# Performance work log

Measured on AMD Instinct MI355X. Metric: run time of the kernel, lower is better.

Reference implementation:

```python
import jax, jax.numpy as jnp
import numpy as np

B, S, D, H = 2, 2048, 1024, 16
HEAD_DIM = D // H
MAX_REL = 64  # max_relative_position in source


def setup_inputs() -> dict:
    key = jax.random.key(0)
    ks = jax.random.split(key, 8)
    std = 0.02
    return {
        "query": jax.random.normal(ks[0], (B, S, D), jnp.float32),
        "key": jax.random.normal(ks[1], (B, S, D), jnp.float32),
        "value": jax.random.normal(ks[2], (B, S, D), jnp.float32),
        "attention_mask": jnp.zeros((B, 1, 1, S), jnp.float32),
        "Wq": jax.random.normal(ks[3], (D, D), jnp.float32) * std,
        "bq": jnp.zeros((D,), jnp.float32),
        "Wk": jax.random.normal(ks[4], (D, D), jnp.float32) * std,
        "bk": jnp.zeros((D,), jnp.float32),
        "Wv": jax.random.normal(ks[5], (D, D), jnp.float32) * std,
        "bv": jnp.zeros((D,), jnp.float32),
        "rel_table": jax.random.normal(ks[6], (2 * MAX_REL + 1, HEAD_DIM), jnp.float32) * std,
    }


def _split_heads(x, b):
    # [B,S,D] -> [B,H,S,d]
    return x.reshape(b, -1, H, HEAD_DIM).transpose(0, 2, 1, 3)


def reference(query, key, value, attention_mask, Wq, bq, Wk, bk, Wv, bv, rel_table):
    b, s, _ = query.shape
    q = _split_heads(query @ Wq + bq, b)   # [B,H,S,d]
    k = _split_heads(key @ Wk + bk, b)
    v = _split_heads(value @ Wv + bv, b)

    scores = jnp.einsum("bhqd,bhkd->bhqk", q, k)  # [B,H,S,S]

    # relative-position key bias: rel_k[q_idx, k_idx] = table[clip(k-q)+MAX_REL]
    idx = jnp.arange(s)
    dist = jnp.clip(idx[None, :] - idx[:, None], -MAX_REL, MAX_REL) + MAX_REL  # [S,S]
    rel_k = rel_table[dist]  # [S,S,d]
    scores = scores + jnp.einsum("bhqd,qkd->bhqk", q, rel_k)

    scores = scores / jnp.sqrt(jnp.asarray(HEAD_DIM, scores.dtype))
    scores = scores + attention_mask  # additive mask, broadcast [B,1,1,S]

    probs = jax.nn.softmax(scores, axis=-1)  # dropout is identity (p=0 / eval)
    ctx = jnp.einsum("bhqk,bhkd->bhqd", probs, v)
    ctx = ctx.transpose(0, 2, 1, 3).reshape(b, s, H * HEAD_DIM)
    return ctx
```

## Files before the change

kernel.cpp:

```cpp
#include <hip/hip_runtime.h>
#include <hip/hip_bf16.h>

#define BB 2
#define SS 2048
#define DD 1024
#define HH 16
#define HD 64
#define NREL 129
#define LOG2E 1.4426950408889634f
#define SCALEQ (LOG2E / 8.0f)
#define KVB 131072l

typedef short s8v __attribute__((ext_vector_type(8)));
typedef short s4v __attribute__((ext_vector_type(4)));
typedef float f4 __attribute__((ext_vector_type(4)));

#define MFMA_BF16 __builtin_amdgcn_mfma_f32_16x16x32_bf16

__device__ __forceinline__ float bf2f(unsigned short u) {
  union { unsigned int i; float f; } x; x.i = ((unsigned int)u) << 16; return x.f;
}
__device__ __forceinline__ unsigned short f2bf(float f) {
  union { float f; unsigned int i; } x; x.f = f;
  unsigned int r = x.i + 0x7fffu + ((x.i >> 16) & 1u);
  return (unsigned short)(r >> 16);
}
__device__ __forceinline__ unsigned int pk2bf(float a, float b) {
  union { __hip_bfloat162 h2; unsigned int u; } c;
  c.h2 = __float22bfloat162_rn(float2{a, b});
  return c.u;
}
__device__ __forceinline__ void gl_lds16(const void* g, void* l) {
  __builtin_amdgcn_global_load_lds(
      (const __attribute__((address_space(1))) unsigned int*)g,
      (__attribute__((address_space(3))) unsigned int*)l, 16, 0, 0);
}

__global__ __launch_bounds__(256) void cvt_x(
    const float* __restrict__ xq, const float* __restrict__ xk,
    const float* __restrict__ xv, unsigned short* __restrict__ xb) {
  const int z = blockIdx.y;
  const float* in = (z == 0) ? xq : (z == 1) ? xk : xv;
  unsigned short* out = xb + (long)z * 4096 * DD;
  const long i = ((long)blockIdx.x * 256 + threadIdx.x) * 8;
  f4 a = *(const f4*)(in + i);
  f4 b = *(const f4*)(in + i + 4);
  unsigned int u[4];
  u[0] = pk2bf(a[0], a[1]); u[1] = pk2bf(a[2], a[3]);
  u[2] = pk2bf(b[0], b[1]); u[3] = pk2bf(b[2], b[3]);
  *(s8v*)(out + i) = *(s8v*)u;
}

__global__ __launch_bounds__(256) void cvt_w(
    const float* __restrict__ Wq, const float* __restrict__ Wk,
    const float* __restrict__ Wv, unsigned short* __restrict__ WTt) {
  __shared__ unsigned short tile[64][72];
  const int z = blockIdx.z;
  const float* in = (z == 0) ? Wq : (z == 1) ? Wk : Wv;
  unsigned short* out = WTt + (long)z * 1048576;
  const int c0 = blockIdx.x * 64, r0 = blockIdx.y * 64;
  const int t = threadIdx.x;
  const int r = t >> 2;
  #pragma unroll
  for (int j = 0; j < 4; ++j) {
    int cc = (t & 3) * 16 + j * 4;
    f4 v = *(const f4*)(in + (long)(r0 + r) * DD + c0 + cc);
    #pragma unroll
    for (int e = 0; e < 4; ++e) tile[r][cc + e] = f2bf(v[e]);
  }
  __syncthreads();
  const int c = t >> 2;
  #pragma unroll
  for (int h = 0; h < 2; ++h) {
    int r8 = (t & 3) + 4 * h;
    unsigned short vals[8];
    #pragma unroll
    for (int j = 0; j < 8; ++j) vals[j] = tile[r8 * 8 + j][c];
    int n = c0 + c, kb = r0 + r8 * 8;
    long off = ((long)(n >> 7) * 131072) + ((kb >> 6) * 8192) +
               (((kb & 63) >> 3) * 1024) + ((n & 127) * 8);
    *(s8v*)(out + off) = *(s8v*)vals;
  }
}

__global__ __launch_bounds__(256, 4) void proj_gemm(
    const unsigned short* __restrict__ Xb, const unsigned short* __restrict__ WTt,
    const float* __restrict__ bq, const float* __restrict__ bk,
    const float* __restrict__ bv,
    unsigned short* __restrict__ qbuf, unsigned short* __restrict__ ktile,
    unsigned short* __restrict__ vtile) {
  __shared__ __align__(16) unsigned short wt[8][128][8];
  unsigned short* wtf = &wt[0][0][0];
  const int z = blockIdx.z;
  const unsigned short* X = Xb + (long)z * 4096 * DD;
  const unsigned short* WTz = WTt + (long)z * 1048576;
  const float* bias = (z == 0) ? bq : (z == 1) ? bk : bv;

  const int n0 = blockIdx.x * 128, m0 = blockIdx.y * 128;
  const int t = threadIdx.x, w = t >> 6, l = t & 63;
  const int lm = l & 15, qd = l >> 4;

  f4 acc[8][2];
  #pragma unroll
  for (int i = 0; i < 8; ++i) { acc[i][0] = (f4)0.0f; acc[i][1] = (f4)0.0f; }

  const unsigned short* x0 = X + (long)(m0 + w * 32 + lm) * DD;
  const unsigned short* x1 = x0 + 16 * DD;
  const unsigned short* wtile0 = WTz + (long)(n0 >> 7) * 131072;

  for (int k0 = 0; k0 < DD; k0 += 64) {
    __syncthreads();
    const unsigned short* tb = wtile0 + (k0 >> 6) * 8192;
    #pragma unroll
    for (int i = 0; i < 4; ++i) {
      int idx = w * 4 + i;
      gl_lds16(tb + idx * 512 + l * 8, wtf + idx * 512);
    }
    s8v a00 = *(const s8v*)(x0 + k0 + qd * 8);
    s8v a01 = *(const s8v*)(x0 + k0 + 32 + qd * 8);
    s8v a10 = *(const s8v*)(x1 + k0 + qd * 8);
    s8v a11 = *(const s8v*)(x1 + k0 + 32 + qd * 8);
    asm volatile("s_waitcnt vmcnt(0)" ::: "memory");
    __syncthreads();
    #pragma unroll
    for (int cb = 0; cb < 8; ++cb) {
      s8v b0 = *(const s8v*)&wt[qd][cb * 16 + lm][0];
      s8v b1 = *(const s8v*)&wt[4 + qd][cb * 16 + lm][0];
      acc[cb][0] = MFMA_BF16(a00, b0, acc[cb][0], 0, 0, 0);
      acc[cb][0] = MFMA_BF16(a01, b1, acc[cb][0], 0, 0, 0);
      acc[cb][1] = MFMA_BF16(a10, b0, acc[cb][1], 0, 0, 0);
      acc[cb][1] = MFMA_BF16(a11, b1, acc[cb][1], 0, 0, 0);
    }
  }
  if (z == 0) {
    #pragma unroll
    for (int cb = 0; cb < 8; ++cb) {
      int n = n0 + cb * 16 + lm;
      float bvv = bias[n];
      int hh = n >> 6, d = n & 63;
      #pragma unroll
      for (int ms = 0; ms < 2; ++ms) {
        #pragma unroll
        for (int r = 0; r < 4; ++r) {
          int m = m0 + w * 32 + ms * 16 + qd * 4 + r;
          int bidx = m >> 11, s = m & (SS - 1);
          qbuf[((long)(bidx * HH + hh) * SS + s) * HD + d] =
              f2bf((acc[cb][ms][r] + bvv) * SCALEQ);
        }
      }
    }
  } else if (z == 1) {
    #pragma unroll
    for (int cb = 0; cb < 8; ++cb) {
      int n = n0 + cb * 16 + lm;
      float bvv = bias[n];
      int hh = n >> 6, d = n & 63;
      int c = d >> 3, e = d & 7;
      #pragma unroll
      for (int ms = 0; ms < 2; ++ms) {
        #pragma unroll
        for (int r = 0; r < 4; ++r) {
          int m = m0 + w * 32 + ms * 16 + qd * 4 + r;
          int bidx = m >> 11, s = m & (SS - 1);
          long bh = bidx * HH + hh;
          ktile[bh * KVB + (s >> 6) * 4096 + c * 512 + (s & 63) * 8 + e] =
              f2bf(acc[cb][ms][r] + bvv);
        }
      }
    }
  } else {
    #pragma unroll
    for (int cb = 0; cb < 8; ++cb) {
      int n = n0 + cb * 16 + lm;
      float bvv = bias[n];
      int hh = n >> 6, d = n & 63;
      #pragma unroll
      for (int ms = 0; ms < 2; ++ms) {
        int m = m0 + w * 32 + ms * 16 + qd * 4;
        int bidx = m >> 11, s = m & (SS - 1);
        long bh = bidx * HH + hh;
        unsigned short o4[4];
        #pragma unroll
        for (int r = 0; r < 4; ++r) o4[r] = f2bf(acc[cb][ms][r] + bvv);
        *(s4v*)&vtile[bh * KVB + (s >> 6) * 4096 + ((s & 63) >> 3) * 512 +
                      d * 8 + (s & 7)] = *(s4v*)o4;
      }
    }
  }
}

__global__ __launch_bounds__(256, 2) void attn(
    const unsigned short* __restrict__ qb, const unsigned short* __restrict__ ktile,
    const unsigned short* __restrict__ vtile, const float* __restrict__ tableF,
    const float* __restrict__ maskF, float* __restrict__ out) {
  __shared__ __align__(16) unsigned short ks[2][8][64][8];
  __shared__ __align__(16) unsigned short vs[2][8][64][8];
  __shared__ __align__(16) unsigned short qr2[NREL][66];
  __shared__ __align__(16) unsigned short pbuf[4][16][40];
  __shared__ float mk[SS];

  const int bh = blockIdx.y, b = bh >> 4, h = bh & 15;
  const int q0 = blockIdx.x * 64;
  const int t = threadIdx.x, w = t >> 6, l = t & 63;
  const int lm = l & 15, qd = l >> 4;

  const unsigned short* kkb = ktile + (long)bh * KVB;
  const unsigned short* vvb = vtile + (long)bh * KVB;

  #pragma unroll
  for (int i = 0; i < 2; ++i) {
    int c = 2 * w + i;
    gl_lds16(kkb + c * 512 + l * 8, &ks[0][c][0][0]);
    gl_lds16(vvb + c * 512 + l * 8, &vs[0][c][0][0]);
  }

  {
    const float* mrow = maskF + b * SS;
    f4 m0v = *(const f4*)(mrow + t * 8);
    f4 m1v = *(const f4*)(mrow + t * 8 + 4);
    #pragma unroll
    for (int e = 0; e < 4; ++e) {
      mk[t * 8 + e] = m0v[e] * LOG2E;
      mk[t * 8 + 4 + e] = m1v[e] * LOG2E;
    }
  }

  const unsigned short* qrow = qb + ((long)bh * SS + q0 + w * 16 + lm) * HD;
  const s8v qa0 = *(const s8v*)(qrow + qd * 8);
  const s8v qa1 = *(const s8v*)(qrow + 32 + qd * 8);

  #pragma unroll
  for (int cb = 0; cb < 9; ++cb) {
    int dist = cb * 16 + lm;
    int dc = dist > NREL - 1 ? NREL - 1 : dist;
    const float* trow = tableF + dc * HD;
    f4 t0 = *(const f4*)(trow + qd * 8);
    f4 t1 = *(const f4*)(trow + qd * 8 + 4);
    f4 t2 = *(const f4*)(trow + 32 + qd * 8);
    f4 t3 = *(const f4*)(trow + 32 + qd * 8 + 4);
    unsigned int tb[8];
    tb[0] = pk2bf(t0[0], t0[1]); tb[1] = pk2bf(t0[2], t0[3]);
    tb[2] = pk2bf(t1[0], t1[1]); tb[3] = pk2bf(t1[2], t1[3]);
    tb[4] = pk2bf(t2[0], t2[1]); tb[5] = pk2bf(t2[2], t2[3]);
    tb[6] = pk2bf(t3[0], t3[1]); tb[7] = pk2bf(t3[2], t3[3]);
    s8v b0 = *(s8v*)tb, b1 = *(s8v*)(tb + 4);
    f4 c = MFMA_BF16(qa0, b0, (f4)0.0f, 0, 0, 0);
    c = MFMA_BF16(qa1, b1, c, 0, 0, 0);
    if (dist <= NREL - 1) {
      #pragma unroll
      for (int r = 0; r < 4; ++r)
        qr2[dist][w * 16 + qd * 4 + r] = f2bf(c[r]);
    }
  }
  asm volatile("s_waitcnt vmcnt(0)" ::: "memory");
  __syncthreads();

  const int qcol = w * 16 + lm;
  const float bLo = bf2f(qr2[0][qcol]);
  const float bHi = bf2f(qr2[128][qcol]);

  float m_ = -1e30f, l_ = 0.0f;
  f4 c4[4];
  #pragma unroll
  for (int i = 0; i < 4; ++i) c4[i] = (f4)0.0f;

  for (int rr = 0; rr < 32; ++rr) {
    const int kk = rr << 6;
    const int buf = rr & 1;
    if (rr < 31) {
      const int nb = buf ^ 1;
      const unsigned short* kg = kkb + (rr + 1) * 4096;
      const unsigned short* vg = vvb + (rr + 1) * 4096;
      #pragma unroll
      for (int i = 0; i < 2; ++i) {
        int c = 2 * w + i;
        gl_lds16(kg + c * 512 + l * 8, &ks[nb][c][0][0]);
        gl_lds16(vg + c * 512 + l * 8, &vs[nb][c][0][0]);
      }
    }
    f4 st[4];
    #pragma unroll
    for (int tt = 0; tt < 4; ++tt) {
      s8v k0v = *(const s8v*)&ks[buf][qd][tt * 16 + lm][0];
      s8v k1v = *(const s8v*)&ks[buf][4 + qd][tt * 16 + lm][0];
      st[tt] = MFMA_BF16(k0v, qa0, (f4)0.0f, 0, 0, 0);
      st[tt] = MFMA_BF16(k1v, qa1, st[tt], 0, 0, 0);
    }
    float z[16];
    const int kband = kk - q0;
    if (kband >= 128) {
      #pragma unroll
      for (int tt = 0; tt < 4; ++tt) {
        f4 mv = *(const f4*)&mk[kk + tt * 16 + qd * 4];
        #pragma unroll
        for (int r = 0; r < 4; ++r) z[tt * 4 + r] = st[tt][r] + bHi + mv[r];
      }
    } else if (kband <= -128) {
      #pragma unroll
      for (int tt = 0; tt < 4; ++tt) {
        f4 mv = *(const f4*)&mk[kk + tt * 16 + qd * 4];
        #pragma unroll
        for (int r = 0; r < 4; ++r) z[tt * 4 + r] = st[tt][r] + bLo + mv[r];
      }
    } else {
      const int dbb = kband - qcol + 64 + qd * 4;
      #pragma unroll
      for (int tt = 0; tt < 4; ++tt) {
        f4 mv = *(const f4*)&mk[kk + tt * 16 + qd * 4];
        #pragma unroll
        for (int r = 0; r < 4; ++r) {
          int d = dbb + tt * 16 + r;
          d = d < 0 ? 0 : (d > 128 ? 128 : d);
          z[tt * 4 + r] = st[tt][r] + bf2f(qr2[d][qcol]) + mv[r];
        }
      }
    }
    float tm = z[0];
    #pragma unroll
    for (int i = 1; i < 16; ++i) tm = fmaxf(tm, z[i]);
    tm = fmaxf(tm, __shfl_xor(tm, 16));
    tm = fmaxf(tm, __shfl_xor(tm, 32));
    float mn = fmaxf(m_, tm);
    float alpha = __builtin_amdgcn_exp2f(m_ - mn);
    m_ = mn;
    float p[16];
    #pragma unroll
    for (int i = 0; i < 16; ++i) p[i] = __builtin_amdgcn_exp2f(z[i] - mn);
    float ts = 0.0f;
    #pragma unroll
    for (int i = 0; i < 16; ++i) ts += p[i];
    ts += __shfl_xor(ts, 16);
    ts += __shfl_xor(ts, 32);
    l_ = l_ * alpha + ts;
    #pragma unroll
    for (int db = 0; db < 4; ++db)
      #pragma unroll
      for (int r = 0; r < 4; ++r) c4[db][r] *= alpha;

    *(unsigned int*)&pbuf[w][lm][qd * 4] = pk2bf(p[0], p[1]);
    *(unsigned int*)&pbuf[w][lm][qd * 4 + 2] = pk2bf(p[2], p[3]);
    *(unsigned int*)&pbuf[w][lm][16 + qd * 4] = pk2bf(p[4], p[5]);
    *(unsigned int*)&pbuf[w][lm][16 + qd * 4 + 2] = pk2bf(p[6], p[7]);
    asm volatile("s_waitcnt lgkmcnt(0)" ::: "memory");
    {
      s8v pa = *(const s8v*)&pbuf[w][lm][qd * 8];
      #pragma unroll
      for (int db = 0; db < 4; ++db) {
        s8v va = *(const s8v*)&vs[buf][qd][db * 16 + lm][0];
        c4[db] = MFMA_BF16(va, pa, c4[db], 0, 0, 0);
      }
    }
    *(unsigned int*)&pbuf[w][lm][qd * 4] = pk2bf(p[8], p[9]);
    *(unsigned int*)&pbuf[w][lm][qd * 4 + 2] = pk2bf(p[10], p[11]);
    *(unsigned int*)&pbuf[w][lm][16 + qd * 4] = pk2bf(p[12], p[13]);
    *(unsigned int*)&pbuf[w][lm][16 + qd * 4 + 2] = pk2bf(p[14], p[15]);
    asm volatile("s_waitcnt lgkmcnt(0)" ::: "memory");
    {
      s8v pb = *(const s8v*)&pbuf[w][lm][qd * 8];
      #pragma unroll
      for (int db = 0; db < 4; ++db) {
        s8v vb = *(const s8v*)&vs[buf][4 + qd][db * 16 + lm][0];
        c4[db] = MFMA_BF16(vb, pb, c4[db], 0, 0, 0);
      }
    }
    asm volatile("s_waitcnt vmcnt(0)" ::: "memory");
    __syncthreads();
  }

  const float inv = 1.0f / l_;
  float* obase = out + ((long)b * SS + q0 + qcol) * DD + h * HD;
  #pragma unroll
  for (int db = 0; db < 4; ++db) {
    f4 o;
    #pragma unroll
    for (int r = 0; r < 4; ++r) o[r] = c4[db][r] * inv;
    *(f4*)(obase + db * 16 + qd * 4) = o;
  }
}

extern "C" void kernel_launch(void* const* d_in, const int* in_sizes, int n_in,
                              void* d_out, int out_size, void* d_ws, size_t ws_size,
                              hipStream_t stream) {
  const float* query = (const float*)d_in[0];
  const float* key   = (const float*)d_in[1];
  const float* value = (const float*)d_in[2];
  const float* mask  = (const float*)d_in[3];
  const float* Wq    = (const float*)d_in[4];
  const float* bq    = (const float*)d_in[5];
  const float* Wk    = (const float*)d_in[6];
  const float* bk    = (const float*)d_in[7];
  const float* Wv    = (const float*)d_in[8];
  const float* bv    = (const float*)d_in[9];
  const float* table = (const float*)d_in[10];

  char* ws = (char*)d_ws;
  unsigned short* WTt   = (unsigned short*)(ws);
  unsigned short* Xb    = (unsigned short*)(ws + (8l << 20));
  unsigned short* qbuf  = (unsigned short*)(ws + (32l << 20));
  unsigned short* ktile = (unsigned short*)(ws + (40l << 20));
  unsigned short* vtile = (unsigned short*)(ws + (48l << 20));

  cvt_x<<<dim3(2048, 3, 1), 256, 0, stream>>>(query, key, value, Xb);

  cvt_w<<<dim3(16, 16, 3), 256, 0, stream>>>(Wq, Wk, Wv, WTt);

  proj_gemm<<<dim3(8, 32, 3), 256, 0, stream>>>(Xb, WTt, bq, bk, bv,
                                                qbuf, ktile, vtile);

  attn<<<dim3(32, 32, 1), 256, 0, stream>>>(qbuf, ktile, vtile, table, mask,
                                            (float*)d_out);
}
```

Measured before the change: 258.1 us.

## Process two 16-row query tiles per wave to reuse K/V fragments

Each wave now handles 32 query rows instead of 16, so the attention block covers 128 queries and the grid halves. K and V fragments read from LDS are reused across both query sub-tiles, which halves K/V global and LDS traffic per query and amortizes the loop sync overhead. The cost is more registers per thread (two accumulator sets and two score arrays), a larger relative-bias LDS table, and only 512 blocks, which may reduce occupancy and latency hiding.

New measurement: 234.9 us. 1.1x faster.

```diff
diff --git a/kernel.cpp b/kernel.cpp
--- a/kernel.cpp
+++ b/kernel.cpp
@@ -195,14 +195,16 @@
     const float* __restrict__ maskF, float* __restrict__ out) {
   __shared__ __align__(16) unsigned short ks[2][8][64][8];
   __shared__ __align__(16) unsigned short vs[2][8][64][8];
-  __shared__ __align__(16) unsigned short qr2[NREL][66];
+  __shared__ __align__(16) unsigned short qr2[NREL][130];
   __shared__ __align__(16) unsigned short pbuf[4][16][40];
   __shared__ float mk[SS];
 
   const int bh = blockIdx.y, b = bh >> 4, h = bh & 15;
-  const int q0 = blockIdx.x * 64;
+  const int q0 = blockIdx.x * 128;
   const int t = threadIdx.x, w = t >> 6, l = t & 63;
   const int lm = l & 15, qd = l >> 4;
+  const int qw = q0 + w * 32;
+  const int qc0 = w * 32 + lm, qc1 = qc0 + 16;
 
   const unsigned short* kkb = ktile + (long)bh * KVB;
   const unsigned short* vvb = vtile + (long)bh * KVB;
@@ -225,9 +227,11 @@
     }
   }
 
-  const unsigned short* qrow = qb + ((long)bh * SS + q0 + w * 16 + lm) * HD;
+  const unsigned short* qrow = qb + ((long)bh * SS + qw + lm) * HD;
   const s8v qa0 = *(const s8v*)(qrow + qd * 8);
   const s8v qa1 = *(const s8v*)(qrow + 32 + qd * 8);
+  const s8v qb0 = *(const s8v*)(qrow + 16 * HD + qd * 8);
+  const s8v qb1 = *(const s8v*)(qrow + 16 * HD + 32 + qd * 8);
 
   #pragma unroll
   for (int cb = 0; cb < 9; ++cb) {
@@ -244,25 +248,28 @@
     tb[4] = pk2bf(t2[0], t2[1]); tb[5] = pk2bf(t2[2], t2[3]);
     tb[6] = pk2bf(t3[0], t3[1]); tb[7] = pk2bf(t3[2], t3[3]);
     s8v b0 = *(s8v*)tb, b1 = *(s8v*)(tb + 4);
-    f4 c = MFMA_BF16(qa0, b0, (f4)0.0f, 0, 0, 0);
-    c = MFMA_BF16(qa1, b1, c, 0, 0, 0);
+    f4 c0 = MFMA_BF16(qa0, b0, (f4)0.0f, 0, 0, 0);
+    c0 = MFMA_BF16(qa1, b1, c0, 0, 0, 0);
+    f4 c1 = MFMA_BF16(qb0, b0, (f4)0.0f, 0, 0, 0);
+    c1 = MFMA_BF16(qb1, b1, c1, 0, 0, 0);
     if (dist <= NREL - 1) {
       #pragma unroll
-      for (int r = 0; r < 4; ++r)
-        qr2[dist][w * 16 + qd * 4 + r] = f2bf(c[r]);
+      for (int r = 0; r < 4; ++r) {
+        qr2[dist][w * 32 + qd * 4 + r] = f2bf(c0[r]);
+        qr2[dist][w * 32 + 16 + qd * 4 + r] = f2bf(c1[r]);
+      }
     }
   }
   asm volatile("s_waitcnt vmcnt(0)" ::: "memory");
   __syncthreads();
 
-  const int qcol = w * 16 + lm;
-  const float bLo = bf2f(qr2[0][qcol]);
-  const float bHi = bf2f(qr2[128][qcol]);
-
-  float m_ = -1e30f, l_ = 0.0f;
-  f4 c4[4];
-  #pragma unroll
-  for (int i = 0; i < 4; ++i) c4[i] = (f4)0.0f;
+  const float bLo0 = bf2f(qr2[0][qc0]), bHi0 = bf2f(qr2[128][qc0]);
+  const float bLo1 = bf2f(qr2[0][qc1]), bHi1 = bf2f(qr2[128][qc1]);
+
+  float m0_ = -1e30f, l0_ = 0.0f, m1_ = -1e30f, l1_ = 0.0f;
+  f4 c40[4], c41[4];
+  #pragma unroll
+  for (int i = 0; i < 4; ++i) { c40[i] = (f4)0.0f; c41[i] = (f4)0.0f; }
 
   for (int rr = 0; rr < 32; ++rr) {
     const int kk = rr << 6;
@@ -278,103 +285,156 @@
         gl_lds16(vg + c * 512 + l * 8, &vs[nb][c][0][0]);
       }
     }
-    f4 st[4];
+    f4 st0[4], st1[4];
     #pragma unroll
     for (int tt = 0; tt < 4; ++tt) {
       s8v k0v = *(const s8v*)&ks[buf][qd][tt * 16 + lm][0];
       s8v k1v = *(const s8v*)&ks[buf][4 + qd][tt * 16 + lm][0];
-      st[tt] = MFMA_BF16(k0v, qa0, (f4)0.0f, 0, 0, 0);
-      st[tt] = MFMA_BF16(k1v, qa1, st[tt], 0, 0, 0);
-    }
-    float z[16];
-    const int kband = kk - q0;
-    if (kband >= 128) {
+      st0[tt] = MFMA_BF16(k0v, qa0, (f4)0.0f, 0, 0, 0);
+      st0[tt] = MFMA_BF16(k1v, qa1, st0[tt], 0, 0, 0);
+      st1[tt] = MFMA_BF16(k0v, qb0, (f4)0.0f, 0, 0, 0);
+      st1[tt] = MFMA_BF16(k1v, qb1, st1[tt], 0, 0, 0);
+    }
+    float z0[16], z1[16];
+    const int kw = kk - qw;
+    if (kw >= 96) {
       #pragma unroll
       for (int tt = 0; tt < 4; ++tt) {
         f4 mv = *(const f4*)&mk[kk + tt * 16 + qd * 4];
         #pragma unroll
-        for (int r = 0; r < 4; ++r) z[tt * 4 + r] = st[tt][r] + bHi + mv[r];
-      }
-    } else if (kband <= -128) {
+        for (int r = 0; r < 4; ++r) {
+          z0[tt * 4 + r] = st0[tt][r] + bHi0 + mv[r];
+          z1[tt * 4 + r] = st1[tt][r] + bHi1 + mv[r];
+        }
+      }
+    } else if (kw <= -128) {
       #pragma unroll
       for (int tt = 0; tt < 4; ++tt) {
         f4 mv = *(const f4*)&mk[kk + tt * 16 + qd * 4];
         #pragma unroll
-        for (int r = 0; r < 4; ++r) z[tt * 4 + r] = st[tt][r] + bLo + mv[r];
+        for (int r = 0; r < 4; ++r) {
+          z0[tt * 4 + r] = st0[tt][r] + bLo0 + mv[r];
+          z1[tt * 4 + r] = st1[tt][r] + bLo1 + mv[r];
+        }
       }
     } else {
-      const int dbb = kband - qcol + 64 + qd * 4;
+      const int db0 = kw - lm + 64 + qd * 4;
       #pragma unroll
       for (int tt = 0; tt < 4; ++tt) {
         f4 mv = *(const f4*)&mk[kk + tt * 16 + qd * 4];
         #pragma unroll
         for (int r = 0; r < 4; ++r) {
-          int d = dbb + tt * 16 + r;
-          d = d < 0 ? 0 : (d > 128 ? 128 : d);
-          z[tt * 4 + r] = st[tt][r] + bf2f(qr2[d][qcol]) + mv[r];
+          int du = db0 + tt * 16 + r;
+          int d0 = du < 0 ? 0 : (du > 128 ? 128 : du);
+          int d1 = du - 16; d1 = d1 < 0 ? 0 : (d1 > 128 ? 128 : d1);
+          z0[tt * 4 + r] = st0[tt][r] + bf2f(qr2[d0][qc0]) + mv[r];
+          z1[tt * 4 + r] = st1[tt][r] + bf2f(qr2[d1][qc1]) + mv[r];
         }
       }
     }
-    float tm = z[0];
-    #pragma unroll
-    for (int i = 1; i < 16; ++i) tm = fmaxf(tm, z[i]);
-    tm = fmaxf(tm, __shfl_xor(tm, 16));
-    tm = fmaxf(tm, __shfl_xor(tm, 32));
-    float mn = fmaxf(m_, tm);
-    float alpha = __builtin_amdgcn_exp2f(m_ - mn);
-    m_ = mn;
-    float p[16];
-    #pragma unroll
-    for (int i = 0; i < 16; ++i) p[i] = __builtin_amdgcn_exp2f(z[i] - mn);
-    float ts = 0.0f;
-    #pragma unroll
-    for (int i = 0; i < 16; ++i) ts += p[i];
-    ts += __shfl_xor(ts, 16);
-    ts += __shfl_xor(ts, 32);
-    l_ = l_ * alpha + ts;
+    float tm0 = z0[0], tm1 = z1[0];
+    #pragma unroll
+    for (int i = 1; i < 16; ++i) {
+      tm0 = fmaxf(tm0, z0[i]);
+      tm1 = fmaxf(tm1, z1[i]);
+    }
+    tm0 = fmaxf(tm0, __shfl_xor(tm0, 16));
+    tm0 = fmaxf(tm0, __shfl_xor(tm0, 32));
+    tm1 = fmaxf(tm1, __shfl_xor(tm1, 16));
+    tm1 = fmaxf(tm1, __shfl_xor(tm1, 32));
+    float mn0 = fmaxf(m0_, tm0), mn1 = fmaxf(m1_, tm1);
+    float al0 = __builtin_amdgcn_exp2f(m0_ - mn0);
+    float al1 = __builtin_amdgcn_exp2f(m1_ - mn1);
+    m0_ = mn0; m1_ = mn1;
+    float s0 = 0.0f, s1 = 0.0f;
+    #pragma unroll
+    for (int i = 0; i < 16; ++i) {
+      z0[i] = __builtin_amdgcn_exp2f(z0[i] - mn0); s0 += z0[i];
+      z1[i] = __builtin_amdgcn_exp2f(z1[i] - mn1); s1 += z1[i];
+    }
+    s0 += __shfl_xor(s0, 16);
+    s0 += __shfl_xor(s0, 32);
+    s1 += __shfl_xor(s1, 16);
+    s1 += __shfl_xor(s1, 32);
+    l0_ = l0_ * al0 + s0; l1_ = l1_ * al1 + s1;
     #pragma unroll
     for (int db = 0; db < 4; ++db)
       #pragma unroll
-      for (int r = 0; r < 4; ++r) c4[db][r] *= alpha;
-
-    *(unsigned int*)&pbuf[w][lm][qd * 4] = pk2bf(p[0], p[1]);
-    *(unsigned int*)&pbuf[w][lm][qd * 4 + 2] = pk2bf(p[2], p[3]);
-    *(unsigned int*)&pbuf[w][lm][16 + qd * 4] = pk2bf(p[4], p[5]);
-    *(unsigned int*)&pbuf[w][lm][16 + qd * 4 + 2] = pk2bf(p[6], p[7]);
-    asm volatile("s_waitcnt lgkmcnt(0)" ::: "memory");
+      for (int r = 0; r < 4; ++r) { c40[db][r] *= al0; c41[db][r] *= al1; }
+
     {
-      s8v pa = *(const s8v*)&pbuf[w][lm][qd * 8];
-      #pragma unroll
-      for (int db = 0; db < 4; ++db) {
-        s8v va = *(const s8v*)&vs[buf][qd][db * 16 + lm][0];
-        c4[db] = MFMA_BF16(va, pa, c4[db], 0, 0, 0);
-      }
-    }
-    *(unsigned int*)&pbuf[w][lm][qd * 4] = pk2bf(p[8], p[9]);
-    *(unsigned int*)&pbuf[w][lm][qd * 4 + 2] = pk2bf(p[10], p[11]);
-    *(unsigned int*)&pbuf[w][lm][16 + qd * 4] = pk2bf(p[12], p[13]);
-    *(unsigned int*)&pbuf[w][lm][16 + qd * 4 + 2] = pk2bf(p[14], p[15]);
-    asm volatile("s_waitcnt lgkmcnt(0)" ::: "memory");
+      s8v va[4];
+      #pragma unroll
+      for (int db = 0; db < 4; ++db)
+        va[db] = *(const s8v*)&vs[buf][qd][db * 16 + lm][0];
+      *(unsigned int*)&pbuf[w][lm][qd * 4] = pk2bf(z0[0], z0[1]);
+      *(unsigned int*)&pbuf[w][lm][qd * 4 + 2] = pk2bf(z0[2], z0[3]);
+      *(unsigned int*)&pbuf[w][lm][16 + qd * 4] = pk2bf(z0[4], z0[5]);
+      *(unsigned int*)&pbuf[w][lm][16 + qd * 4 + 2] = pk2bf(z0[6], z0[7]);
+      asm volatile("s_waitcnt lgkmcnt(0)" ::: "memory");
+      {
+        s8v pa = *(const s8v*)&pbuf[w][lm][qd * 8];
+        #pragma unroll
+        for (int db = 0; db < 4; ++db)
+          c40[db] = MFMA_BF16(va[db], pa, c40[db], 0, 0, 0);
+      }
+      *(unsigned int*)&pbuf[w][lm][qd * 4] = pk2bf(z1[0], z1[1]);
+      *(unsigned int*)&pbuf[w][lm][qd * 4 + 2] = pk2bf(z1[2], z1[3]);
+      *(unsigned int*)&pbuf[w][lm][16 + qd * 4] = pk2bf(z1[4], z1[5]);
+      *(unsigned int*)&pbuf[w][lm][16 + qd * 4 + 2] = pk2bf(z1[6], z1[7]);
+      asm volatile("s_waitcnt lgkmcnt(0)" ::: "memory");
+      {
+        s8v pa = *(const s8v*)&pbuf[w][lm][qd * 8];
+        #pragma unroll
+        for (int db = 0; db < 4; ++db)
+          c41[db] = MFMA_BF16(va[db], pa, c41[db], 0, 0, 0);
+      }
+    }
     {
-      s8v pb = *(const s8v*)&pbuf[w][lm][qd * 8];
-      #pragma unroll
-      for (int db = 0; db < 4; ++db) {
-        s8v vb = *(const s8v*)&vs[buf][4 + qd][db * 16 + lm][0];
-        c4[db] = MFMA_BF16(vb, pb, c4[db], 0, 0, 0);
+      s8v vb[4];
+      #pragma unroll
+      for (int db = 0; db < 4; ++db)
+        vb[db] = *(const s8v*)&vs[buf][4 + qd][db * 16 + lm][0];
+      *(unsigned int*)&pbuf[w][lm][qd * 4] = pk2bf(z0[8], z0[9]);
+      *(unsigned int*)&pbuf[w][lm][qd * 4 + 2] = pk2bf(z0[10], z0[11]);
+      *(unsigned int*)&pbuf[w][lm][16 + qd * 4] = pk2bf(z0[12], z0[13]);
+      *(unsigned int*)&pbuf[w][lm][16 + qd * 4 + 2] = pk2bf(z0[14], z0[15]);
+      asm volatile("s_waitcnt lgkmcnt(0)" ::: "memory");
+      {
+        s8v pb = *(const s8v*)&pbuf[w][lm][qd * 8];
+        #pragma unroll
+        for (int db = 0; db < 4; ++db)
+          c40[db] = MFMA_BF16(vb[db], pb, c40[db], 0, 0, 0);
+      }
+      *(unsigned int*)&pbuf[w][lm][qd * 4] = pk2bf(z1[8], z1[9]);
+      *(unsigned int*)&pbuf[w][lm][qd * 4 + 2] = pk2bf(z1[10], z1[11]);
+      *(unsigned int*)&pbuf[w][lm][16 + qd * 4] = pk2bf(z1[12], z1[13]);
+      *(unsigned int*)&pbuf[w][lm][16 + qd * 4 + 2] = pk2bf(z1[14], z1[15]);
+      asm volatile("s_waitcnt lgkmcnt(0)" ::: "memory");
+      {
+        s8v pb = *(const s8v*)&pbuf[w][lm][qd * 8];
+        #pragma unroll
+        for (int db = 0; db < 4; ++db)
+          c41[db] = MFMA_BF16(vb[db], pb, c41[db], 0, 0, 0);
       }
     }
     asm volatile("s_waitcnt vmcnt(0)" ::: "memory");
     __syncthreads();
   }
 
-  const float inv = 1.0f / l_;
-  float* obase = out + ((long)b * SS + q0 + qcol) * DD + h * HD;
+  const float inv0 = 1.0f / l0_, inv1 = 1.0f / l1_;
+  float* ob0 = out + ((long)b * SS + q0 + qc0) * DD + h * HD;
+  float* ob1 = out + ((long)b * SS + q0 + qc1) * DD + h * HD;
   #pragma unroll
   for (int db = 0; db < 4; ++db) {
-    f4 o;
-    #pragma unroll
-    for (int r = 0; r < 4; ++r) o[r] = c4[db][r] * inv;
-    *(f4*)(obase + db * 16 + qd * 4) = o;
+    f4 o0, o1;
+    #pragma unroll
+    for (int r = 0; r < 4; ++r) {
+      o0[r] = c40[db][r] * inv0;
+      o1[r] = c41[db][r] * inv1;
+    }
+    *(f4*)(ob0 + db * 16 + qd * 4) = o0;
+    *(f4*)(ob1 + db * 16 + qd * 4) = o1;
   }
 }
 
@@ -407,6 +467,6 @@
   proj_gemm<<<dim3(8, 32, 3), 256, 0, stream>>>(Xb, WTt, bq, bk, bv,
                                                 qbuf, ktile, vtile);
 
-  attn<<<dim3(32, 32, 1), 256, 0, stream>>>(qbuf, ktile, vtile, table, mask,
+  attn<<<dim3(16, 32, 1), 256, 0, stream>>>(qbuf, ktile, vtile, table, mask,
                                             (float*)d_out);
 }
```

## Process two query sub-tiles per wave and load K/V directly into registers

Applied to the files above, without the earlier changes.

Each attention block now covers 128 queries instead of 64, so each wave handles two 16-row query sub-tiles that share every K/V fragment. K/V tiles are no longer staged through LDS with a per-iteration barrier; each wave loads them from global memory straight into registers, double-buffered by a manually unrolled loop. The aim is to halve K/V traffic per query and remove LDS staging and __syncthreads. In exchange there are far more live registers (16 K/V fragments plus two sets of accumulators), which risks spills or lower occupancy, and the grid is half the size.

New measurement: 348.5 us. 1.35x slower.

```diff
diff --git a/kernel.cpp b/kernel.cpp
--- a/kernel.cpp
+++ b/kernel.cpp
@@ -189,30 +189,157 @@
   }
 }
 
+
+#define LOADKV(RR, K, V) do {                                                \
+    const unsigned short* kg_ = kkb + (RR) * 4096;                           \
+    const unsigned short* vg_ = vvb + (RR) * 4096;                           \
+    _Pragma("unroll")                                                        \
+    for (int tt = 0; tt < 4; ++tt) {                                         \
+      K[tt]     = *(const s8v*)(kg_ + qd * 512 + (tt * 16 + lm) * 8);        \
+      K[4 + tt] = *(const s8v*)(kg_ + (4 + qd) * 512 + (tt * 16 + lm) * 8);  \
+      V[tt]     = *(const s8v*)(vg_ + qd * 512 + (tt * 16 + lm) * 8);        \
+      V[4 + tt] = *(const s8v*)(vg_ + (4 + qd) * 512 + (tt * 16 + lm) * 8);  \
+    }                                                                        \
+  } while (0)
+
+#define ATTN_STEP(RR, CK, CV, NK, NV, DONEXT) do {                           \
+    const int kk = (RR) << 6;                                                \
+    if (DONEXT) { LOADKV((RR) + 1, NK, NV); }                                \
+    f4 st0[4], st1[4];                                                       \
+    _Pragma("unroll")                                                        \
+    for (int tt = 0; tt < 4; ++tt) {                                         \
+      st0[tt] = MFMA_BF16(CK[tt], qa0, (f4)0.0f, 0, 0, 0);                   \
+      st0[tt] = MFMA_BF16(CK[4 + tt], qa1, st0[tt], 0, 0, 0);                \
+      st1[tt] = MFMA_BF16(CK[tt], qb0, (f4)0.0f, 0, 0, 0);                   \
+      st1[tt] = MFMA_BF16(CK[4 + tt], qb1, st1[tt], 0, 0, 0);                \
+    }                                                                        \
+    float z0[16], z1[16];                                                    \
+    const int kw = kk - qw;                                                  \
+    if (kw >= 96) {                                                          \
+      _Pragma("unroll")                                                      \
+      for (int tt = 0; tt < 4; ++tt) {                                       \
+        f4 mv = *(const f4*)&mk[kk + tt * 16 + qd * 4];                      \
+        _Pragma("unroll")                                                    \
+        for (int r = 0; r < 4; ++r) {                                        \
+          z0[tt * 4 + r] = st0[tt][r] + bHi0 + mv[r];                        \
+          z1[tt * 4 + r] = st1[tt][r] + bHi1 + mv[r];                        \
+        }                                                                    \
+      }                                                                      \
+    } else if (kw <= -128) {                                                 \
+      _Pragma("unroll")                                                      \
+      for (int tt = 0; tt < 4; ++tt) {                                       \
+        f4 mv = *(const f4*)&mk[kk + tt * 16 + qd * 4];                      \
+        _Pragma("unroll")                                                    \
+        for (int r = 0; r < 4; ++r) {                                        \
+          z0[tt * 4 + r] = st0[tt][r] + bLo0 + mv[r];                        \
+          z1[tt * 4 + r] = st1[tt][r] + bLo1 + mv[r];                        \
+        }                                                                    \
+      }                                                                      \
+    } else {                                                                 \
+      const int db0 = kw - lm + 64 + qd * 4;                                 \
+      _Pragma("unroll")                                                      \
+      for (int tt = 0; tt < 4; ++tt) {                                       \
+        f4 mv = *(const f4*)&mk[kk + tt * 16 + qd * 4];                      \
+        _Pragma("unroll")                                                    \
+        for (int r = 0; r < 4; ++r) {                                        \
+          int du = db0 + tt * 16 + r;                                        \
+          int d0 = du < 0 ? 0 : (du > 128 ? 128 : du);                       \
+          int d1 = du - 16; d1 = d1 < 0 ? 0 : (d1 > 128 ? 128 : d1);         \
+          z0[tt * 4 + r] = st0[tt][r] + bf2f(qr2[d0][qc0]) + mv[r];          \
+          z1[tt * 4 + r] = st1[tt][r] + bf2f(qr2[d1][qc1]) + mv[r];          \
+        }                                                                    \
+      }                                                                      \
+    }                                                                        \
+    float tm0 = z0[0], tm1 = z1[0];                                          \
+    _Pragma("unroll")                                                        \
+    for (int i = 1; i < 16; ++i) {                                           \
+      tm0 = fmaxf(tm0, z0[i]);                                               \
+      tm1 = fmaxf(tm1, z1[i]);                                               \
+    }                                                                        \
+    tm0 = fmaxf(tm0, __shfl_xor(tm0, 16));                                   \
+    tm0 = fmaxf(tm0, __shfl_xor(tm0, 32));                                   \
+    tm1 = fmaxf(tm1, __shfl_xor(tm1, 16));                                   \
+    tm1 = fmaxf(tm1, __shfl_xor(tm1, 32));                                   \
+    float mn0 = fmaxf(m0_, tm0), mn1 = fmaxf(m1_, tm1);                      \
+    float al0 = __builtin_amdgcn_exp2f(m0_ - mn0);                           \
+    float al1 = __builtin_amdgcn_exp2f(m1_ - mn1);                           \
+    m0_ = mn0; m1_ = mn1;                                                    \
+    float s0 = 0.0f, s1 = 0.0f;                                              \
+    _Pragma("unroll")                                                        \
+    for (int i = 0; i < 16; ++i) {                                           \
+      z0[i] = __builtin_amdgcn_exp2f(z0[i] - mn0); s0 += z0[i];              \
+      z1[i] = __builtin_amdgcn_exp2f(z1[i] - mn1); s1 += z1[i];              \
+    }                                                                        \
+    s0 += __shfl_xor(s0, 16);                                                \
+    s0 += __shfl_xor(s0, 32);                                                \
+    s1 += __shfl_xor(s1, 16);                                                \
+    s1 += __shfl_xor(s1, 32);                                                \
+    l0_ = l0_ * al0 + s0; l1_ = l1_ * al1 + s1;                              \
+    _Pragma("unroll")                                                        \
+    for (int db = 0; db < 4; ++db)                                           \
+      _Pragma("unroll")                                                      \
+      for (int r = 0; r < 4; ++r) { c40[db][r] *= al0; c41[db][r] *= al1; }  \
+     \
+    *(unsigned int*)&pb0[w][lm][qd * 4]          = pk2bf(z0[0], z0[1]);      \
+    *(unsigned int*)&pb0[w][lm][qd * 4 + 2]      = pk2bf(z0[2], z0[3]);      \
+    *(unsigned int*)&pb0[w][lm][16 + qd * 4]     = pk2bf(z0[4], z0[5]);      \
+    *(unsigned int*)&pb0[w][lm][16 + qd * 4 + 2] = pk2bf(z0[6], z0[7]);      \
+    *(unsigned int*)&pb1[w][lm][qd * 4]          = pk2bf(z1[0], z1[1]);      \
+    *(unsigned int*)&pb1[w][lm][qd * 4 + 2]      = pk2bf(z1[2], z1[3]);      \
+    *(unsigned int*)&pb1[w][lm][16 + qd * 4]     = pk2bf(z1[4], z1[5]);      \
+    *(unsigned int*)&pb1[w][lm][16 + qd * 4 + 2] = pk2bf(z1[6], z1[7]);      \
+    asm volatile("s_waitcnt lgkmcnt(0)" ::: "memory");                       \
+    {                                                                        \
+      s8v pa0 = *(const s8v*)&pb0[w][lm][qd * 8];                            \
+      s8v pa1 = *(const s8v*)&pb1[w][lm][qd * 8];                            \
+      _Pragma("unroll")                                                      \
+      for (int db = 0; db < 4; ++db) {                                       \
+        c40[db] = MFMA_BF16(CV[db], pa0, c40[db], 0, 0, 0);                  \
+        c41[db] = MFMA_BF16(CV[db], pa1, c41[db], 0, 0, 0);                  \
+      }                                                                      \
+    }                                                                        \
+                                               \
+    *(unsigned int*)&pb0[w][lm][qd * 4]          = pk2bf(z0[8], z0[9]);      \
+    *(unsigned int*)&pb0[w][lm][qd * 4 + 2]      = pk2bf(z0[10], z0[11]);    \
+    *(unsigned int*)&pb0[w][lm][16 + qd * 4]     = pk2bf(z0[12], z0[13]);    \
+    *(unsigned int*)&pb0[w][lm][16 + qd * 4 + 2] = pk2bf(z0[14], z0[15]);    \
+    *(unsigned int*)&pb1[w][lm][qd * 4]          = pk2bf(z1[8], z1[9]);      \
+    *(unsigned int*)&pb1[w][lm][qd * 4 + 2]      = pk2bf(z1[10], z1[11]);    \
+    *(unsigned int*)&pb1[w][lm][16 + qd * 4]     = pk2bf(z1[12], z1[13]);    \
+    *(unsigned int*)&pb1[w][lm][16 + qd * 4 + 2] = pk2bf(z1[14], z1[15]);    \
+    asm volatile("s_waitcnt lgkmcnt(0)" ::: "memory");                       \
+    {                                                                        \
+      s8v pb0v = *(const s8v*)&pb0[w][lm][qd * 8];                           \
+      s8v pb1v = *(const s8v*)&pb1[w][lm][qd * 8];                           \
+      _Pragma("unroll")                                                      \
+      for (int db = 0; db < 4; ++db) {                                       \
+        c40[db] = MFMA_BF16(CV[4 + db], pb0v, c40[db], 0, 0, 0);             \
+        c41[db] = MFMA_BF16(CV[4 + db], pb1v, c41[db], 0, 0, 0);             \
+      }                                                                      \
+    }                                                                        \
+  } while (0)
+
 __global__ __launch_bounds__(256, 2) void attn(
     const unsigned short* __restrict__ qb, const unsigned short* __restrict__ ktile,
     const unsigned short* __restrict__ vtile, const float* __restrict__ tableF,
     const float* __restrict__ maskF, float* __restrict__ out) {
-  __shared__ __align__(16) unsigned short ks[2][8][64][8];
-  __shared__ __align__(16) unsigned short vs[2][8][64][8];
-  __shared__ __align__(16) unsigned short qr2[NREL][66];
-  __shared__ __align__(16) unsigned short pbuf[4][16][40];
+  __shared__ __align__(16) unsigned short qr2[NREL][130];
+  __shared__ __align__(16) unsigned short pb0[4][16][40];
+  __shared__ __align__(16) unsigned short pb1[4][16][40];
   __shared__ float mk[SS];
 
   const int bh = blockIdx.y, b = bh >> 4, h = bh & 15;
-  const int q0 = blockIdx.x * 64;
+  const int q0 = blockIdx.x * 128;
   const int t = threadIdx.x, w = t >> 6, l = t & 63;
   const int lm = l & 15, qd = l >> 4;
+  const int qw = q0 + w * 32;
+  const int qc0 = w * 32 + lm, qc1 = qc0 + 16;
 
   const unsigned short* kkb = ktile + (long)bh * KVB;
   const unsigned short* vvb = vtile + (long)bh * KVB;
 
-  #pragma unroll
-  for (int i = 0; i < 2; ++i) {
-    int c = 2 * w + i;
-    gl_lds16(kkb + c * 512 + l * 8, &ks[0][c][0][0]);
-    gl_lds16(vvb + c * 512 + l * 8, &vs[0][c][0][0]);
-  }
+  s8v K0[8], V0[8], K1[8], V1[8];
+  LOADKV(0, K0, V0);
 
   {
     const float* mrow = maskF + b * SS;
@@ -225,9 +352,11 @@
     }
   }
 
-  const unsigned short* qrow = qb + ((long)bh * SS + q0 + w * 16 + lm) * HD;
+  const unsigned short* qrow = qb + ((long)bh * SS + qw + lm) * HD;
   const s8v qa0 = *(const s8v*)(qrow + qd * 8);
   const s8v qa1 = *(const s8v*)(qrow + 32 + qd * 8);
+  const s8v qb0 = *(const s8v*)(qrow + 16 * HD + qd * 8);
+  const s8v qb1 = *(const s8v*)(qrow + 16 * HD + 32 + qd * 8);
 
   #pragma unroll
   for (int cb = 0; cb < 9; ++cb) {
@@ -244,137 +373,46 @@
     tb[4] = pk2bf(t2[0], t2[1]); tb[5] = pk2bf(t2[2], t2[3]);
     tb[6] = pk2bf(t3[0], t3[1]); tb[7] = pk2bf(t3[2], t3[3]);
     s8v b0 = *(s8v*)tb, b1 = *(s8v*)(tb + 4);
-    f4 c = MFMA_BF16(qa0, b0, (f4)0.0f, 0, 0, 0);
-    c = MFMA_BF16(qa1, b1, c, 0, 0, 0);
+    f4 c0 = MFMA_BF16(qa0, b0, (f4)0.0f, 0, 0, 0);
+    c0 = MFMA_BF16(qa1, b1, c0, 0, 0, 0);
+    f4 c1 = MFMA_BF16(qb0, b0, (f4)0.0f, 0, 0, 0);
+    c1 = MFMA_BF16(qb1, b1, c1, 0, 0, 0);
     if (dist <= NREL - 1) {
       #pragma unroll
-      for (int r = 0; r < 4; ++r)
-        qr2[dist][w * 16 + qd * 4 + r] = f2bf(c[r]);
-    }
-  }
-  asm volatile("s_waitcnt vmcnt(0)" ::: "memory");
+      for (int r = 0; r < 4; ++r) {
+        qr2[dist][w * 32 + qd * 4 + r] = f2bf(c0[r]);
+        qr2[dist][w * 32 + 16 + qd * 4 + r] = f2bf(c1[r]);
+      }
+    }
+  }
   __syncthreads();
 
-  const int qcol = w * 16 + lm;
-  const float bLo = bf2f(qr2[0][qcol]);
-  const float bHi = bf2f(qr2[128][qcol]);
-
-  float m_ = -1e30f, l_ = 0.0f;
-  f4 c4[4];
-  #pragma unroll
-  for (int i = 0; i < 4; ++i) c4[i] = (f4)0.0f;
-
-  for (int rr = 0; rr < 32; ++rr) {
-    const int kk = rr << 6;
-    const int buf = rr & 1;
-    if (rr < 31) {
-      const int nb = buf ^ 1;
-      const unsigned short* kg = kkb + (rr + 1) * 4096;
-      const unsigned short* vg = vvb + (rr + 1) * 4096;
-      #pragma unroll
-      for (int i = 0; i < 2; ++i) {
-        int c = 2 * w + i;
-        gl_lds16(kg + c * 512 + l * 8, &ks[nb][c][0][0]);
-        gl_lds16(vg + c * 512 + l * 8, &vs[nb][c][0][0]);
-      }
-    }
-    f4 st[4];
-    #pragma unroll
-    for (int tt = 0; tt < 4; ++tt) {
-      s8v k0v = *(const s8v*)&ks[buf][qd][tt * 16 + lm][0];
-      s8v k1v = *(const s8v*)&ks[buf][4 + qd][tt * 16 + lm][0];
-      st[tt] = MFMA_BF16(k0v, qa0, (f4)0.0f, 0, 0, 0);
-      st[tt] = MFMA_BF16(k1v, qa1, st[tt], 0, 0, 0);
-    }
-    float z[16];
-    const int kband = kk - q0;
-    if (kband >= 128) {
-      #pragma unroll
-      for (int tt = 0; tt < 4; ++tt) {
-        f4 mv = *(const f4*)&mk[kk + tt * 16 + qd * 4];
-        #pragma unroll
-        for (int r = 0; r < 4; ++r) z[tt * 4 + r] = st[tt][r] + bHi + mv[r];
-      }
-    } else if (kband <= -128) {
-      #pragma unroll
-      for (int tt = 0; tt < 4; ++tt) {
-        f4 mv = *(const f4*)&mk[kk + tt * 16 + qd * 4];
-        #pragma unroll
-        for (int r = 0; r < 4; ++r) z[tt * 4 + r] = st[tt][r] + bLo + mv[r];
-      }
-    } else {
-      const int dbb = kband - qcol + 64 + qd * 4;
-      #pragma unroll
-      for (int tt = 0; tt < 4; ++tt) {
-        f4 mv = *(const f4*)&mk[kk + tt * 16 + qd * 4];
-        #pragma unroll
-        for (int r = 0; r < 4; ++r) {
-          int d = dbb + tt * 16 + r;
-          d = d < 0 ? 0 : (d > 128 ? 128 : d);
-          z[tt * 4 + r] = st[tt][r] + bf2f(qr2[d][qcol]) + mv[r];
-        }
-      }
-    }
-    float tm = z[0];
-    #pragma unroll
-    for (int i = 1; i < 16; ++i) tm = fmaxf(tm, z[i]);
-    tm = fmaxf(tm, __shfl_xor(tm, 16));
-    tm = fmaxf(tm, __shfl_xor(tm, 32));
-    float mn = fmaxf(m_, tm);
-    float alpha = __builtin_amdgcn_exp2f(m_ - mn);
-    m_ = mn;
-    float p[16];
-    #pragma unroll
-    for (int i = 0; i < 16; ++i) p[i] = __builtin_amdgcn_exp2f(z[i] - mn);
-    float ts = 0.0f;
-    #pragma unroll
-    for (int i = 0; i < 16; ++i) ts += p[i];
-    ts += __shfl_xor(ts, 16);
-    ts += __shfl_xor(ts, 32);
-    l_ = l_ * alpha + ts;
-    #pragma unroll
-    for (int db = 0; db < 4; ++db)
-      #pragma unroll
-      for (int r = 0; r < 4; ++r) c4[db][r] *= alpha;
-
-    *(unsigned int*)&pbuf[w][lm][qd * 4] = pk2bf(p[0], p[1]);
-    *(unsigned int*)&pbuf[w][lm][qd * 4 + 2] = pk2bf(p[2], p[3]);
-    *(unsigned int*)&pbuf[w][lm][16 + qd * 4] = pk2bf(p[4], p[5]);
-    *(unsigned int*)&pbuf[w][lm][16 + qd * 4 + 2] = pk2bf(p[6], p[7]);
-    asm volatile("s_waitcnt lgkmcnt(0)" ::: "memory");
-    {
-      s8v pa = *(const s8v*)&pbuf[w][lm][qd * 8];
-      #pragma unroll
-      for (int db = 0; db < 4; ++db) {
-        s8v va = *(const s8v*)&vs[buf][qd][db * 16 + lm][0];
-        c4[db] = MFMA_BF16(va, pa, c4[db], 0, 0, 0);
-      }
-    }
-    *(unsigned int*)&pbuf[w][lm][qd * 4] = pk2bf(p[8], p[9]);
-    *(unsigned int*)&pbuf[w][lm][qd * 4 + 2] = pk2bf(p[10], p[11]);
-    *(unsigned int*)&pbuf[w][lm][16 + qd * 4] = pk2bf(p[12], p[13]);
-    *(unsigned int*)&pbuf[w][lm][16 + qd * 4 + 2] = pk2bf(p[14], p[15]);
-    asm volatile("s_waitcnt lgkmcnt(0)" ::: "memory");
-    {
-      s8v pb = *(const s8v*)&pbuf[w][lm][qd * 8];
-      #pragma unroll
-      for (int db = 0; db < 4; ++db) {
-        s8v vb = *(const s8v*)&vs[buf][4 + qd][db * 16 + lm][0];
-        c4[db] = MFMA_BF16(vb, pb, c4[db], 0, 0, 0);
-      }
-    }
-    asm volatile("s_waitcnt vmcnt(0)" ::: "memory");
-    __syncthreads();
-  }
-
-  const float inv = 1.0f / l_;
-  float* obase = out + ((long)b * SS + q0 + qcol) * DD + h * HD;
+  const float bLo0 = bf2f(qr2[0][qc0]), bHi0 = bf2f(qr2[128][qc0]);
+  const float bLo1 = bf2f(qr2[0][qc1]), bHi1 = bf2f(qr2[128][qc1]);
+
+  float m0_ = -1e30f, l0_ = 0.0f, m1_ = -1e30f, l1_ = 0.0f;
+  f4 c40[4], c41[4];
+  #pragma unroll
+  for (int i = 0; i < 4; ++i) { c40[i] = (f4)0.0f; c41[i] = (f4)0.0f; }
+
+  for (int rp = 0; rp < 16; ++rp) {
+    ATTN_STEP(2 * rp, K0, V0, K1, V1, true);
+    ATTN_STEP(2 * rp + 1, K1, V1, K0, V0, (rp < 15));
+  }
+
+  const float inv0 = 1.0f / l0_, inv1 = 1.0f / l1_;
+  float* ob0 = out + ((long)b * SS + q0 + qc0) * DD + h * HD;
+  float* ob1 = out + ((long)b * SS + q0 + qc1) * DD + h * HD;
   #pragma unroll
   for (int db = 0; db < 4; ++db) {
-    f4 o;
-    #pragma unroll
-    for (int r = 0; r < 4; ++r) o[r] = c4[db][r] * inv;
-    *(f4*)(obase + db * 16 + qd * 4) = o;
+    f4 o0, o1;
+    #pragma unroll
+    for (int r = 0; r < 4; ++r) {
+      o0[r] = c40[db][r] * inv0;
+      o1[r] = c41[db][r] * inv1;
+    }
+    *(f4*)(ob0 + db * 16 + qd * 4) = o0;
+    *(f4*)(ob1 + db * 16 + qd * 4) = o1;
   }
 }
 
@@ -407,6 +445,6 @@
   proj_gemm<<<dim3(8, 32, 3), 256, 0, stream>>>(Xb, WTt, bq, bk, bv,
                                                 qbuf, ktile, vtile);
 
-  attn<<<dim3(32, 32, 1), 256, 0, stream>>>(qbuf, ktile, vtile, table, mask,
+  attn<<<dim3(16, 32, 1), 256, 0, stream>>>(qbuf, ktile, vtile, table, mask,
                                             (float*)d_out);
 }
```
